# Kernel tuning notes

Measured on AMD Instinct MI355X. Metric: run time of the kernel, lower is better.

Reference implementation:

```python
import jax, jax.numpy as jnp
import numpy as np

B, S, D = 16, 2048, 128


def setup_inputs() -> dict:
    key = jax.random.key(0)
    k1, k2, k3, k4 = jax.random.split(key, 4)
    return {
        "query": jax.random.normal(k1, (B, S, D), dtype=jnp.float32),
        "key": jax.random.normal(k2, (B, S, D), dtype=jnp.float32),
        "value": jax.random.normal(k3, (B, S, D), dtype=jnp.float32),
        "scale_factor": jax.random.normal(k4, (1, S, S), dtype=jnp.float32),
        "dropout_p": 0,
    }


def reference(query, key, value, scale_factor, dropout_p):
    # qk = Q K^T  -> [B, S, S]
    qk = jnp.einsum("bqd,bkd->bqk", query, key)
    # elementwise scale matrix (broadcast over batch), then row softmax
    scaled_qk = qk * scale_factor
    softmax_qk = jax.nn.softmax(scaled_qk, axis=-1)
    # dropout_p == 0 -> identity (eval-mode / deterministic baseline)
    # output = P V -> [B, S, D]
    return jnp.einsum("bqk,bkd->bqd", softmax_qk, value)
```

## Files before the change

### kernel.cpp

```cpp
#include <hip/hip_runtime.h>
#include <hip/hip_bf16.h>

#define SS 2048
#define DD 128
#define KT 64
#define NT (SS / KT)

typedef float floatx4 __attribute__((ext_vector_type(4)));
typedef __bf16 bf16x8 __attribute__((ext_vector_type(8)));
typedef unsigned short u16x4 __attribute__((ext_vector_type(4)));
typedef unsigned short u16x8 __attribute__((ext_vector_type(8)));

__device__ __forceinline__ int kcol_perm(int d) {
    return ((d >> 5) << 5) | (((d & 15) >> 2) << 3) | (((d >> 4) & 1) << 2) | (d & 3);
}

__device__ __forceinline__ unsigned short bfbits(float x) {
    __bf16 h = (__bf16)x;
    return __builtin_bit_cast(unsigned short, h);
}

__global__ __launch_bounds__(256, 1)
void attn_scaled_kernel(const float* __restrict__ Q, const float* __restrict__ K,
                        const float* __restrict__ V, const float* __restrict__ Sc,
                        float* __restrict__ Out) {
    __shared__ __align__(16) unsigned short Khi[KT * DD];
    __shared__ __align__(16) unsigned short Klo[KT * DD];
    __shared__ __align__(16) unsigned short Vt[DD * KT];

    const int t    = threadIdx.x;
    const int w    = t >> 6;
    const int lane = t & 63;
    const int lq   = lane & 15;
    const int qg   = lane >> 4;

    const int p     = blockIdx.x;
    const int wid   = ((p & 7) << 5) + (p >> 3);
    const int batch = wid >> 4;
    const int q0    = (wid & 15) << 7;

    const float* Qb = Q + (size_t)batch * SS * DD;
    const float* Kb = K + (size_t)batch * SS * DD;
    const float* Vb = V + (size_t)batch * SS * DD;

    const int srow = t >> 5;
    const int c4   = (t & 31) << 2;
    const int kw0  = srow * 128 + (kcol_perm(c4) ^ ((srow & 7) << 3));
    const float* Kp = Kb + (size_t)srow * DD + c4;

    const int vd   = ((w & 1) << 6) + lane;
    const int vkv  = w >> 1;
    const int vswz = (vd & 7) << 3;
    const float* Vp = Vb + vd;

#define STAGE_K(I, KV) do {                                           \
        float ks_[4] = {(KV).x, (KV).y, (KV).z, (KV).w};              \
        u16x4 hh_, ll_;                                               \
        _Pragma("unroll")                                             \
        for (int e_ = 0; e_ < 4; ++e_) {                              \
            __bf16 hb_ = (__bf16)ks_[e_];                             \
            __bf16 lb_ = (__bf16)(ks_[e_] - (float)hb_);              \
            hh_[e_] = __builtin_bit_cast(unsigned short, hb_);        \
            ll_[e_] = __builtin_bit_cast(unsigned short, lb_);        \
        }                                                             \
        *(u16x4*)&Khi[kw0 + 1024 * (I)] = hh_;                        \
        *(u16x4*)&Klo[kw0 + 1024 * (I)] = ll_;                        \
    } while (0)

#define STAGE_V(I, VPI) do {                                          \
        u16x8 vv_;                                                    \
        _Pragma("unroll")                                             \
        for (int e_ = 0; e_ < 8; ++e_) vv_[e_] = bfbits((VPI)[e_]);   \
        *(u16x8*)&Vt[((vd << 6) + (vkv << 5) + ((I) << 3)) ^ vswz] = vv_; \
    } while (0)

#define LOAD_V(I, VPI, BASE) do {                                     \
        _Pragma("unroll")                                             \
        for (int h_ = 0; h_ < 2; ++h_)                                \
            _Pragma("unroll")                                         \
            for (int j_ = 0; j_ < 4; ++j_)                            \
                (VPI)[h_ * 4 + j_] =                                  \
                    Vp[(BASE) + (size_t)((vkv << 5) + ((I) << 2) + (h_ << 4) + j_) * DD]; \
    } while (0)

    const int qrow0 = q0 + (w << 5) + lq;
    bf16x8 qh[2][4], ql[2][4];
#pragma unroll
    for (int h2 = 0; h2 < 2; ++h2) {
        const float* Qr = Qb + (size_t)(qrow0 + 16 * h2) * DD;
#pragma unroll
        for (int ds = 0; ds < 4; ++ds) {
#pragma unroll
            for (int h = 0; h < 2; ++h) {
                float4 qv = *(const float4*)(Qr + (qg << 2) + (h << 4) + (ds << 5));
                float xs[4] = {qv.x, qv.y, qv.z, qv.w};
#pragma unroll
                for (int e = 0; e < 4; ++e) {
                    __bf16 hb = (__bf16)xs[e];
                    __bf16 lb = (__bf16)(xs[e] - (float)hb);
                    qh[h2][ds][h * 4 + e] = hb;
                    ql[h2][ds][h * 4 + e] = lb;
                }
            }
        }
    }

    const float* ScRow0 = Sc + (size_t)qrow0 * SS;

    float4 scur[2][4];
    {
        float4 kn[8];
        float  vp[4][8];
#pragma unroll
        for (int i = 0; i < 8; ++i) kn[i] = *(const float4*)(Kp + (size_t)(8 * i) * DD);
#pragma unroll
        for (int i = 0; i < 4; ++i) LOAD_V(i, vp[i], 0);
#pragma unroll
        for (int h2 = 0; h2 < 2; ++h2)
#pragma unroll
            for (int g = 0; g < 4; ++g)
                scur[h2][g] = *(const float4*)(ScRow0 + (size_t)(h2 * 16) * SS + g * 16 + (qg << 2));
#pragma unroll
        for (int i = 0; i < 8; ++i) STAGE_K(i, kn[i]);
#pragma unroll
        for (int i = 0; i < 4; ++i) STAGE_V(i, vp[i]);
    }
    __syncthreads();

    floatx4 O[2][8];
#pragma unroll
    for (int h2 = 0; h2 < 2; ++h2)
#pragma unroll
        for (int i = 0; i < 8; ++i) O[h2][i] = (floatx4){0.f, 0.f, 0.f, 0.f};
    float m_run[2] = {-INFINITY, -INFINITY};
    float l_run[2] = {0.f, 0.f};

    for (int kt = 0; kt < NT; ++kt) {
        const int kbase = kt << 6;
        const bool pre = (kt + 1 < NT);
        float4 kn[8], scn[2][4];
        float  vp[4][8];
        if (pre) {
            const size_t off = (size_t)(kbase + KT) * DD;
#pragma unroll
            for (int i = 0; i < 8; ++i)
                kn[i] = *(const float4*)(Kp + off + (size_t)(8 * i) * DD);
#pragma unroll
            for (int i = 0; i < 4; ++i) LOAD_V(i, vp[i], off);
#pragma unroll
            for (int h2 = 0; h2 < 2; ++h2)
#pragma unroll
                for (int g = 0; g < 4; ++g)
                    scn[h2][g] = *(const float4*)(ScRow0 + (size_t)(h2 * 16) * SS
                                                  + kbase + KT + g * 16 + (qg << 2));
        }

        floatx4 st[2][4];
#pragma unroll
        for (int h2 = 0; h2 < 2; ++h2)
#pragma unroll
            for (int g = 0; g < 4; ++g) st[h2][g] = (floatx4){0.f, 0.f, 0.f, 0.f};
        const int sx = (lq & 7) << 3;
        __builtin_amdgcn_s_setprio(1);
#pragma unroll
        for (int ds = 0; ds < 4; ++ds) {
            const int cc = (ds << 5) + (qg << 3);
#pragma unroll
            for (int g = 0; g < 4; ++g) {
                const int b = ((g * 16 + lq) * 128 + cc) ^ sx;
                bf16x8 kh = *(const bf16x8*)&Khi[b];
                bf16x8 kl = *(const bf16x8*)&Klo[b];
#pragma unroll
                for (int h2 = 0; h2 < 2; ++h2) {
                    st[h2][g] = __builtin_amdgcn_mfma_f32_16x16x32_bf16(kh, qh[h2][ds], st[h2][g], 0, 0, 0);
                    st[h2][g] = __builtin_amdgcn_mfma_f32_16x16x32_bf16(kh, ql[h2][ds], st[h2][g], 0, 0, 0);
                    st[h2][g] = __builtin_amdgcn_mfma_f32_16x16x32_bf16(kl, qh[h2][ds], st[h2][g], 0, 0, 0);
                }
            }
        }
        __builtin_amdgcn_s_setprio(0);

        bf16x8 pa[2][2];
#pragma unroll
        for (int h2 = 0; h2 < 2; ++h2) {
            float sv[16];
#pragma unroll
            for (int g = 0; g < 4; ++g) {
                sv[g * 4 + 0] = st[h2][g][0] * scur[h2][g].x;
                sv[g * 4 + 1] = st[h2][g][1] * scur[h2][g].y;
                sv[g * 4 + 2] = st[h2][g][2] * scur[h2][g].z;
                sv[g * 4 + 3] = st[h2][g][3] * scur[h2][g].w;
            }
            float tm = fmaxf(fmaxf(fmaxf(sv[0], sv[1]), fmaxf(sv[2], sv[3])),
                             fmaxf(fmaxf(sv[4], sv[5]), fmaxf(sv[6], sv[7])));
            float tm2 = fmaxf(fmaxf(fmaxf(sv[8], sv[9]), fmaxf(sv[10], sv[11])),
                              fmaxf(fmaxf(sv[12], sv[13]), fmaxf(sv[14], sv[15])));
            tm = fmaxf(tm, tm2);
            tm = fmaxf(tm, __shfl_xor(tm, 16));
            tm = fmaxf(tm, __shfl_xor(tm, 32));
            float mnew  = fmaxf(m_run[h2], tm);
            float alpha = __expf(m_run[h2] - mnew);
            m_run[h2] = mnew;

            float psum = 0.f;
#pragma unroll
            for (int e = 0; e < 4; ++e) {
                float p0 = __expf(sv[e]      - mnew);
                float p1 = __expf(sv[4 + e]  - mnew);
                float p2 = __expf(sv[8 + e]  - mnew);
                float p3 = __expf(sv[12 + e] - mnew);
                psum += (p0 + p1) + (p2 + p3);
                pa[h2][0][e] = (__bf16)p0; pa[h2][0][4 + e] = (__bf16)p1;
                pa[h2][1][e] = (__bf16)p2; pa[h2][1][4 + e] = (__bf16)p3;
            }
            psum += __shfl_xor(psum, 16);
            psum += __shfl_xor(psum, 32);
            l_run[h2] = l_run[h2] * alpha + psum;

            float ar0 = __shfl(alpha, (qg << 2) + 0);
            float ar1 = __shfl(alpha, (qg << 2) + 1);
            float ar2 = __shfl(alpha, (qg << 2) + 2);
            float ar3 = __shfl(alpha, (qg << 2) + 3);
#pragma unroll
            for (int df = 0; df < 8; ++df) {
                O[h2][df][0] *= ar0; O[h2][df][1] *= ar1;
                O[h2][df][2] *= ar2; O[h2][df][3] *= ar3;
            }
        }

        __builtin_amdgcn_s_setprio(1);
#pragma unroll
        for (int df = 0; df < 8; ++df) {
            const int d   = lq + (df << 4);
            const int vb0 = (((d << 6) +      (qg << 3)) ^ sx);
            const int vb1 = (((d << 6) + 32 + (qg << 3)) ^ sx);
            bf16x8 vf0 = *(const bf16x8*)&Vt[vb0];
            bf16x8 vf1 = *(const bf16x8*)&Vt[vb1];
#pragma unroll
            for (int h2 = 0; h2 < 2; ++h2) {
                O[h2][df] = __builtin_amdgcn_mfma_f32_16x16x32_bf16(pa[h2][0], vf0, O[h2][df], 0, 0, 0);
                O[h2][df] = __builtin_amdgcn_mfma_f32_16x16x32_bf16(pa[h2][1], vf1, O[h2][df], 0, 0, 0);
            }
        }
        __builtin_amdgcn_s_setprio(0);

        if (pre) {
            __syncthreads();
#pragma unroll
            for (int i = 0; i < 8; ++i) STAGE_K(i, kn[i]);
#pragma unroll
            for (int i = 0; i < 4; ++i) STAGE_V(i, vp[i]);
#pragma unroll
            for (int h2 = 0; h2 < 2; ++h2)
#pragma unroll
                for (int g = 0; g < 4; ++g) scur[h2][g] = scn[h2][g];
            __syncthreads();
        }
    }

#pragma unroll
    for (int h2 = 0; h2 < 2; ++h2) {
        float inv0 = 1.f / __shfl(l_run[h2], (qg << 2) + 0);
        float inv1 = 1.f / __shfl(l_run[h2], (qg << 2) + 1);
        float inv2 = 1.f / __shfl(l_run[h2], (qg << 2) + 2);
        float inv3 = 1.f / __shfl(l_run[h2], (qg << 2) + 3);
        const size_t obase = ((size_t)batch * SS + (size_t)(q0 + (w << 5) + 16 * h2)) * DD;
#pragma unroll
        for (int df = 0; df < 8; ++df) {
            int d = lq + (df << 4);
            Out[obase + (size_t)((qg << 2) + 0) * DD + d] = O[h2][df][0] * inv0;
            Out[obase + (size_t)((qg << 2) + 1) * DD + d] = O[h2][df][1] * inv1;
            Out[obase + (size_t)((qg << 2) + 2) * DD + d] = O[h2][df][2] * inv2;
            Out[obase + (size_t)((qg << 2) + 3) * DD + d] = O[h2][df][3] * inv3;
        }
    }
#undef STAGE_K
#undef STAGE_V
#undef LOAD_V
}

extern "C" void kernel_launch(void* const* d_in, const int* in_sizes, int n_in,
                              void* d_out, int out_size, void* d_ws, size_t ws_size,
                              hipStream_t stream) {
    const float* q  = (const float*)d_in[0];
    const float* k  = (const float*)d_in[1];
    const float* v  = (const float*)d_in[2];
    const float* sc = (const float*)d_in[3];
    float* out = (float*)d_out;
    hipLaunchKernelGGL(attn_scaled_kernel, dim3(256), dim3(256), 0, stream,
                       q, k, v, sc, out);
}
```

Baseline: 227.7 us.

## Prepack K/V into MFMA-fragment bf16 layout in workspace and read directly from global

Adds a prepack kernel that splits K into hi/lo bf16 and converts V to bf16, storing both in the per-lane MFMA fragment order in the workspace. A new attention kernel then loads fragments straight from global memory with no LDS staging or barriers, uses 64-row query tiles over 512 blocks with two blocks per CU, and raises wave priority around the MFMA sections. This is meant to remove the in-kernel conversion and the LDS round trips. In exchange it adds an extra launch, workspace traffic and global-load latency that is not hidden by double buffering, and it falls back to the old kernel when the workspace is too small.

```diff
diff --git a/kernel.cpp b/kernel.cpp
--- a/kernel.cpp
+++ b/kernel.cpp
@@ -11,6 +11,13 @@
 typedef unsigned short u16x4 __attribute__((ext_vector_type(4)));
 typedef unsigned short u16x8 __attribute__((ext_vector_type(8)));
 
+#define KHI_OFF 0
+#define KLO_OFF 8388608
+#define VW_OFF  16777216
+#define WS_NEED 25165824
+#define KJOB    (1 << 19)
+#define BSTRIDE 262144u
+
 __device__ __forceinline__ int kcol_perm(int d) {
     return ((d >> 5) << 5) | (((d & 15) >> 2) << 3) | (((d >> 4) & 1) << 2) | (d & 3);
 }
@@ -18,6 +25,193 @@
 __device__ __forceinline__ unsigned short bfbits(float x) {
     __bf16 h = (__bf16)x;
     return __builtin_bit_cast(unsigned short, h);
+}
+
+__global__ __launch_bounds__(256)
+void prepack_kernel(const float* __restrict__ K, const float* __restrict__ V,
+                    unsigned short* __restrict__ khi, unsigned short* __restrict__ klo,
+                    unsigned short* __restrict__ vw) {
+    const int tid = blockIdx.x * 256 + threadIdx.x;
+    if (tid < KJOB) {
+        const int lane = tid & 63, g = (tid >> 6) & 3, ds = (tid >> 8) & 3;
+        const int kt = (tid >> 10) & 31, b = tid >> 15;
+        const int lq = lane & 15, qg = lane >> 4;
+        const int key = kt * 64 + g * 16 + lq;
+        const int d0  = 32 * ds + 4 * qg;
+        const float* src = K + ((size_t)(b * SS + key)) * DD + d0;
+        float4 a = *(const float4*)src;
+        float4 c = *(const float4*)(src + 16);
+        float xs[8] = {a.x, a.y, a.z, a.w, c.x, c.y, c.z, c.w};
+        u16x8 hh, ll;
+#pragma unroll
+        for (int j = 0; j < 8; ++j) {
+            __bf16 hb = (__bf16)xs[j];
+            __bf16 lb = (__bf16)(xs[j] - (float)hb);
+            hh[j] = __builtin_bit_cast(unsigned short, hb);
+            ll[j] = __builtin_bit_cast(unsigned short, lb);
+        }
+        *(u16x8*)&khi[(size_t)tid * 8] = hh;
+        *(u16x8*)&klo[(size_t)tid * 8] = ll;
+    } else {
+        const int tv = tid - KJOB;
+        const int d = tv & 127, qg = (tv >> 7) & 3, half = (tv >> 9) & 1;
+        const int kt = (tv >> 10) & 31, b = tv >> 15;
+        u16x8 vv;
+#pragma unroll
+        for (int j = 0; j < 8; ++j) {
+            const int key = kt * 64 + 32 * half + 4 * qg + 16 * (j >> 2) + (j & 3);
+            vv[j] = bfbits(V[((size_t)(b * SS + key)) * DD + d]);
+        }
+        const int df = d >> 4, lq = d & 15;
+        const size_t slot = ((((size_t)(b * 32 + kt) * 2 + half) * 8 + df) * 16 + lq) * 4 + qg;
+        *(u16x8*)&vw[slot * 8] = vv;
+    }
+}
+
+__global__ __launch_bounds__(256, 2)
+void attn_gd_kernel(const float* __restrict__ Q, const float* __restrict__ Sc,
+                    const unsigned short* __restrict__ khi,
+                    const unsigned short* __restrict__ klo,
+                    const unsigned short* __restrict__ vw,
+                    float* __restrict__ Out) {
+    const int t    = threadIdx.x;
+    const int w    = t >> 6;
+    const int lane = t & 63;
+    const int lq   = lane & 15;
+    const int qg   = lane >> 4;
+
+    const int p     = blockIdx.x;
+    const int wid   = ((p & 7) << 6) + (p >> 3);
+    const int batch = wid >> 5;
+    const int q0    = (wid & 31) << 6;
+
+    const int qrow = q0 + (w << 4) + lq;
+    const float* Qr = Q + ((size_t)batch * SS + qrow) * DD;
+    bf16x8 qh[4], ql[4];
+#pragma unroll
+    for (int ds = 0; ds < 4; ++ds) {
+#pragma unroll
+        for (int h = 0; h < 2; ++h) {
+            float4 qv = *(const float4*)(Qr + (qg << 2) + (h << 4) + (ds << 5));
+            float xs[4] = {qv.x, qv.y, qv.z, qv.w};
+#pragma unroll
+            for (int e = 0; e < 4; ++e) {
+                __bf16 hb = (__bf16)xs[e];
+                __bf16 lb = (__bf16)(xs[e] - (float)hb);
+                qh[ds][h * 4 + e] = hb;
+                ql[ds][h * 4 + e] = lb;
+            }
+        }
+    }
+
+    const float* ScRow = Sc + (size_t)qrow * SS;
+
+    floatx4 O[8];
+#pragma unroll
+    for (int i = 0; i < 8; ++i) O[i] = (floatx4){0.f, 0.f, 0.f, 0.f};
+    float m_run = -INFINITY, l_run = 0.f;
+
+    const unsigned kfrag0 = (unsigned)batch * BSTRIDE + (unsigned)lane * 8;
+    const unsigned vfrag0 = (unsigned)batch * BSTRIDE + (unsigned)lq * 32 + (unsigned)qg * 8;
+
+    for (int kt = 0; kt < NT; ++kt) {
+        const int kbase = kt << 6;
+        const unsigned kb = kfrag0 + (unsigned)kt * 8192;
+        const unsigned vb = vfrag0 + (unsigned)kt * 8192;
+
+        floatx4 st[4];
+#pragma unroll
+        for (int g = 0; g < 4; ++g) st[g] = (floatx4){0.f, 0.f, 0.f, 0.f};
+        __builtin_amdgcn_s_setprio(1);
+#pragma unroll
+        for (int ds = 0; ds < 4; ++ds) {
+#pragma unroll
+            for (int g = 0; g < 4; ++g) {
+                const unsigned idx = kb + (unsigned)((ds * 4 + g) * 512);
+                bf16x8 kh = *(const bf16x8*)&khi[idx];
+                bf16x8 kl = *(const bf16x8*)&klo[idx];
+                st[g] = __builtin_amdgcn_mfma_f32_16x16x32_bf16(kh, qh[ds], st[g], 0, 0, 0);
+                st[g] = __builtin_amdgcn_mfma_f32_16x16x32_bf16(kh, ql[ds], st[g], 0, 0, 0);
+                st[g] = __builtin_amdgcn_mfma_f32_16x16x32_bf16(kl, qh[ds], st[g], 0, 0, 0);
+            }
+        }
+        __builtin_amdgcn_s_setprio(0);
+
+        const float* sr = ScRow + kbase;
+        float4 sc0 = *(const float4*)(sr + (qg << 2));
+        float4 sc1 = *(const float4*)(sr + 16 + (qg << 2));
+        float4 sc2 = *(const float4*)(sr + 32 + (qg << 2));
+        float4 sc3 = *(const float4*)(sr + 48 + (qg << 2));
+        float sv[16];
+        sv[0]  = st[0][0] * sc0.x; sv[1]  = st[0][1] * sc0.y;
+        sv[2]  = st[0][2] * sc0.z; sv[3]  = st[0][3] * sc0.w;
+        sv[4]  = st[1][0] * sc1.x; sv[5]  = st[1][1] * sc1.y;
+        sv[6]  = st[1][2] * sc1.z; sv[7]  = st[1][3] * sc1.w;
+        sv[8]  = st[2][0] * sc2.x; sv[9]  = st[2][1] * sc2.y;
+        sv[10] = st[2][2] * sc2.z; sv[11] = st[2][3] * sc2.w;
+        sv[12] = st[3][0] * sc3.x; sv[13] = st[3][1] * sc3.y;
+        sv[14] = st[3][2] * sc3.z; sv[15] = st[3][3] * sc3.w;
+
+        float tm = fmaxf(fmaxf(fmaxf(sv[0], sv[1]), fmaxf(sv[2], sv[3])),
+                         fmaxf(fmaxf(sv[4], sv[5]), fmaxf(sv[6], sv[7])));
+        float tm2 = fmaxf(fmaxf(fmaxf(sv[8], sv[9]), fmaxf(sv[10], sv[11])),
+                          fmaxf(fmaxf(sv[12], sv[13]), fmaxf(sv[14], sv[15])));
+        tm = fmaxf(tm, tm2);
+        tm = fmaxf(tm, __shfl_xor(tm, 16));
+        tm = fmaxf(tm, __shfl_xor(tm, 32));
+        float mnew  = fmaxf(m_run, tm);
+        float alpha = __expf(m_run - mnew);
+        m_run = mnew;
+
+        float psum = 0.f;
+        bf16x8 pa0, pa1;
+#pragma unroll
+        for (int e = 0; e < 4; ++e) {
+            float p0 = __expf(sv[e]      - mnew);
+            float p1 = __expf(sv[4 + e]  - mnew);
+            float p2 = __expf(sv[8 + e]  - mnew);
+            float p3 = __expf(sv[12 + e] - mnew);
+            psum += (p0 + p1) + (p2 + p3);
+            pa0[e] = (__bf16)p0; pa0[4 + e] = (__bf16)p1;
+            pa1[e] = (__bf16)p2; pa1[4 + e] = (__bf16)p3;
+        }
+        psum += __shfl_xor(psum, 16);
+        psum += __shfl_xor(psum, 32);
+        l_run = l_run * alpha + psum;
+
+        float ar0 = __shfl(alpha, (qg << 2) + 0);
+        float ar1 = __shfl(alpha, (qg << 2) + 1);
+        float ar2 = __shfl(alpha, (qg << 2) + 2);
+        float ar3 = __shfl(alpha, (qg << 2) + 3);
+#pragma unroll
+        for (int df = 0; df < 8; ++df) {
+            O[df][0] *= ar0; O[df][1] *= ar1; O[df][2] *= ar2; O[df][3] *= ar3;
+        }
+
+        __builtin_amdgcn_s_setprio(1);
+#pragma unroll
+        for (int df = 0; df < 8; ++df) {
+            bf16x8 vf0 = *(const bf16x8*)&vw[vb + (unsigned)(df * 512)];
+            bf16x8 vf1 = *(const bf16x8*)&vw[vb + 4096u + (unsigned)(df * 512)];
+            O[df] = __builtin_amdgcn_mfma_f32_16x16x32_bf16(pa0, vf0, O[df], 0, 0, 0);
+            O[df] = __builtin_amdgcn_mfma_f32_16x16x32_bf16(pa1, vf1, O[df], 0, 0, 0);
+        }
+        __builtin_amdgcn_s_setprio(0);
+    }
+
+    float inv0 = 1.f / __shfl(l_run, (qg << 2) + 0);
+    float inv1 = 1.f / __shfl(l_run, (qg << 2) + 1);
+    float inv2 = 1.f / __shfl(l_run, (qg << 2) + 2);
+    float inv3 = 1.f / __shfl(l_run, (qg << 2) + 3);
+    const size_t obase = ((size_t)batch * SS + (size_t)(q0 + (w << 4))) * DD;
+#pragma unroll
+    for (int df = 0; df < 8; ++df) {
+        int d = lq + (df << 4);
+        Out[obase + (size_t)((qg << 2) + 0) * DD + d] = O[df][0] * inv0;
+        Out[obase + (size_t)((qg << 2) + 1) * DD + d] = O[df][1] * inv1;
+        Out[obase + (size_t)((qg << 2) + 2) * DD + d] = O[df][2] * inv2;
+        Out[obase + (size_t)((qg << 2) + 3) * DD + d] = O[df][3] * inv3;
+    }
 }
 
 __global__ __launch_bounds__(256, 1)
@@ -287,6 +481,16 @@
     const float* v  = (const float*)d_in[2];
     const float* sc = (const float*)d_in[3];
     float* out = (float*)d_out;
-    hipLaunchKernelGGL(attn_scaled_kernel, dim3(256), dim3(256), 0, stream,
-                       q, k, v, sc, out);
-}
+    if (ws_size >= (size_t)WS_NEED) {
+        unsigned short* khi = (unsigned short*)((char*)d_ws + KHI_OFF);
+        unsigned short* klo = (unsigned short*)((char*)d_ws + KLO_OFF);
+        unsigned short* vw  = (unsigned short*)((char*)d_ws + VW_OFF);
+        hipLaunchKernelGGL(prepack_kernel, dim3(4096), dim3(256), 0, stream,
+                           k, v, khi, klo, vw);
+        hipLaunchKernelGGL(attn_gd_kernel, dim3(512), dim3(256), 0, stream,
+                           q, sc, khi, klo, vw, out);
+    } else {
+        hipLaunchKernelGGL(attn_scaled_kernel, dim3(256), dim3(256), 0, stream,
+                           q, k, v, sc, out);
+    }
+}
```

New measurement: 390.0 us. 1.71x slower.
